# Kernel optimization log

Measured on AMD Instinct MI355X. Metric: run time of the kernel, lower is better.

Reference implementation:

```python
import jax, jax.numpy as jnp
import numpy as np

B, S, DIM, H, HD, K, DEPTH = 2, 2048, 1024, 16, 64, 64, 8
SCALE = 1.0 / np.sqrt(HD)


def _build_cantor_routes(seq_len: int, k: int, depth: int) -> np.ndarray:
    # Vectorized version of CantorAttention._build_cantor_routes
    pos = np.arange(seq_len, dtype=np.float64)
    x = pos / max(1, seq_len - 1)
    x = np.clip(x, 1e-06, 1.0 - 1e-06)
    cantor = np.zeros(seq_len, dtype=np.float64)
    factor = 0.5
    for _ in range(depth):
        x = x * 3.0
        digit = np.floor(x)
        x = x - digit
        cantor += factor * (digit == 2.0)
        factor *= 0.5
    cantor = cantor.astype(np.float32)
    # k nearest positions in Cantor space for each position
    dist = np.abs(cantor[:, None] - cantor[None, :])  # [S, S]
    routes = np.argsort(dist, axis=1, kind='stable')[:, :k]  # [S, k]
    return routes.astype(np.int32)


def setup_inputs() -> dict:
    key = jax.random.key(0)
    k1, k2, k3, k4, k5 = jax.random.split(key, 5)
    s = 1.0 / np.sqrt(DIM)
    return {
        'x': jax.random.normal(k1, (B, S, DIM), dtype=jnp.float32),
        'w_qkv': jax.random.normal(k2, (3 * DIM, DIM), dtype=jnp.float32) * s,
        'b_qkv': jax.random.normal(k3, (3 * DIM,), dtype=jnp.float32) * 0.01,
        'w_out': jax.random.normal(k4, (DIM, DIM), dtype=jnp.float32) * s,
        'b_out': jax.random.normal(k5, (DIM,), dtype=jnp.float32) * 0.01,
        'routes': jnp.asarray(_build_cantor_routes(S, K, DEPTH)),
    }


def reference(x, w_qkv, b_qkv, w_out, b_out, routes):
    b, s, _ = x.shape
    # QKV projection (torch Linear: y = x @ W.T + b)
    qkv = x @ w_qkv.T + b_qkv                       # [B, S, 3*DIM]
    qkv = qkv.reshape(b, s, 3, H, HD).transpose(2, 0, 3, 1, 4)  # [3, B, H, S, HD]
    q, k, v = qkv[0], qkv[1], qkv[2]                # each [B, H, S, HD]
    # Gather k/v at Cantor neighbor routes: [B, H, S, K, HD]
    k_g = jnp.take(k, routes, axis=2)
    v_g = jnp.take(v, routes, axis=2)
    scores = jnp.einsum('bhqd,bhqkd->bhqk', q, k_g) * SCALE
    attn = jax.nn.softmax(scores, axis=-1)
    out = jnp.einsum('bhqk,bhqkd->bhqd', attn, v_g)  # [B, H, S, HD]
    out = out.transpose(0, 2, 1, 3).reshape(b, s, DIM)
    return out @ w_out.T + b_out
```

## Files before the change

kernel.cpp:

```cpp
#include <hip/hip_runtime.h>

#define BQ   2
#define SQ   2048
#define DIMQ 1024
#define HQ   16
#define HDQ  64
#define KQ   64
#define QKV_STRIDE (3 * DIMQ)

typedef __attribute__((ext_vector_type(8))) short short8;
typedef __attribute__((ext_vector_type(4))) float floatx4;

typedef const __attribute__((address_space(1))) unsigned short* gas_t;
typedef __attribute__((address_space(3))) unsigned short* las_t;

__device__ __forceinline__ unsigned short f2b(float f) {
    union { float f; unsigned int u; } x; x.f = f;
    unsigned int r = x.u + 0x7fffu + ((x.u >> 16) & 1u);
    return (unsigned short)(r >> 16);
}
__device__ __forceinline__ float b2f(unsigned short u) {
    union { unsigned int u; float f; } x; x.u = ((unsigned int)u) << 16;
    return x.f;
}

__global__ __launch_bounds__(256) void cast3_f32_bf16(const float* __restrict__ s0, unsigned short* __restrict__ d0, int n0,
                                                      const float* __restrict__ s1, unsigned short* __restrict__ d1, int n1,
                                                      const float* __restrict__ s2, unsigned short* __restrict__ d2, int n2) {
    int i = blockIdx.x * blockDim.x + threadIdx.x;
    const float* s; unsigned short* d;
    if (i < n0)                { s = s0; d = d0; }
    else if (i < n0 + n1)      { s = s1; d = d1; i -= n0; }
    else if (i < n0 + n1 + n2) { s = s2; d = d2; i -= n0 + n1; }
    else return;
    float4 v = ((const float4*)s)[i];
    ushort4 o;
    o.x = f2b(v.x); o.y = f2b(v.y); o.z = f2b(v.z); o.w = f2b(v.w);
    ((ushort4*)d)[i] = o;
}

template <int BM, int BN, typename CT>
__global__ __launch_bounds__(256) void gemm_bf16_nt(const unsigned short* __restrict__ A,
                                                    const unsigned short* __restrict__ B,
                                                    const float* __restrict__ bias,
                                                    CT* __restrict__ C,
                                                    int M, int N, int K) {
    constexpr int MI = BM / 32;
    constexpr int NJ = BN / 32;
    __shared__ unsigned short As[BM * 64];
    __shared__ unsigned short Bs[BN * 64];

    const int tid  = threadIdx.x;
    const int lane = tid & 63;
    const int wv   = tid >> 6;
    const int wm   = (wv >> 1) * (BM / 2);
    const int wn   = (wv & 1) * (BN / 2);
    const int fr   = lane & 15;
    const int fq   = lane >> 4;

    const int m0 = blockIdx.y * BM;
    const int n0 = blockIdx.x * BN;

    floatx4 acc[MI][NJ];
#pragma unroll
    for (int i = 0; i < MI; ++i)
#pragma unroll
        for (int j = 0; j < NJ; ++j) acc[i][j] = (floatx4)(0.f);

    const unsigned short* Ab = A + (size_t)m0 * K;
    const unsigned short* Bb = B + (size_t)n0 * K;

    for (int k0 = 0; k0 < K; k0 += 64) {
#pragma unroll
        for (int c = 0; c < (BM + BN) * 8; c += 256) {
            const int cc = c + tid;
            if (cc < BM * 8) {
                const int row = cc >> 3;
                const int kc  = ((cc & 7) ^ (row & 7)) << 3;
                __builtin_amdgcn_global_load_lds(
                    (gas_t)(Ab + (size_t)row * K + k0 + kc),
                    (las_t)&As[cc * 8], 16, 0, 0);
            } else {
                const int c2  = cc - BM * 8;
                const int row = c2 >> 3;
                const int kc  = ((c2 & 7) ^ (row & 7)) << 3;
                __builtin_amdgcn_global_load_lds(
                    (gas_t)(Bb + (size_t)row * K + k0 + kc),
                    (las_t)&Bs[c2 * 8], 16, 0, 0);
            }
        }
        __syncthreads();

#pragma unroll
        for (int ks = 0; ks < 2; ++ks) {
            short8 af[MI], bf[NJ];
#pragma unroll
            for (int i = 0; i < MI; ++i) {
                const int row = wm + i * 16 + fr;
                const int pos = (ks * 4 + fq) ^ (row & 7);
                af[i] = *(const short8*)&As[row * 64 + pos * 8];
            }
#pragma unroll
            for (int j = 0; j < NJ; ++j) {
                const int row = wn + j * 16 + fr;
                const int pos = (ks * 4 + fq) ^ (row & 7);
                bf[j] = *(const short8*)&Bs[row * 64 + pos * 8];
            }
#pragma unroll
            for (int i = 0; i < MI; ++i)
#pragma unroll
                for (int j = 0; j < NJ; ++j)
                    acc[i][j] = __builtin_amdgcn_mfma_f32_16x16x32_bf16(af[i], bf[j], acc[i][j], 0, 0, 0);
        }
        __syncthreads();
    }

    float bv[NJ];
#pragma unroll
    for (int j = 0; j < NJ; ++j) bv[j] = bias[n0 + wn + j * 16 + fr];
#pragma unroll
    for (int i = 0; i < MI; ++i) {
#pragma unroll
        for (int r = 0; r < 4; ++r) {
            const size_t row = (size_t)(m0 + wm + i * 16 + fq * 4 + r);
#pragma unroll
            for (int j = 0; j < NJ; ++j) {
                const float v = acc[i][j][r] + bv[j];
                if constexpr (sizeof(CT) == 2)
                    C[row * N + n0 + wn + j * 16 + fr] = (CT)f2b(v);
                else
                    C[row * N + n0 + wn + j * 16 + fr] = (CT)v;
            }
        }
    }
}

__global__ __launch_bounds__(256) void attn_kernel(const unsigned short* __restrict__ qkv,
                                                   const int* __restrict__ routes,
                                                   unsigned short* __restrict__ out) {
    __shared__ int   r_s[KQ];
    __shared__ float m_s[128], l_s[128];
    __shared__ float o_part[8][128];

    const int t  = threadIdx.x;
    const int id = blockIdx.x;
    const int bq = (id & 7) * 512 + (id >> 3);
    const int b  = bq >> 11;
    const int q  = bq & 2047;

    if (t < KQ) r_s[t] = routes[q * KQ + t];

    const int g  = t >> 7;
    const int th = t & 127;
    const int h  = th >> 3;
    const int d0 = (t & 7) * 8;

    float qf[8];
    {
        const short8 q8 = *(const short8*)&qkv[((size_t)bq * 3) * DIMQ + h * HDQ + d0];
#pragma unroll
        for (int e = 0; e < 8; ++e) qf[e] = b2f((unsigned short)q8[e]) * 0.18033688011112042f;
    }
    __syncthreads();

    const unsigned short* baseK = qkv + ((size_t)b * SQ * 3 + 1) * DIMQ + h * HDQ + d0;
    const unsigned short* baseV = qkv + ((size_t)b * SQ * 3 + 2) * DIMQ + h * HDQ + d0;

    float s[32];
    short8 kb[4];
#pragma unroll
    for (int i = 0; i < 4; ++i) {
        const size_t roff = (size_t)r_s[i * 2 + g] * QKV_STRIDE;
        kb[i] = *(const short8*)(baseK + roff);
    }
#pragma unroll
    for (int jj = 0; jj < 32; ++jj) {
        const int slot = jj & 3;
        const short8 k8 = kb[slot];
        if (jj + 4 < 32) {
            const size_t roff = (size_t)r_s[(jj + 4) * 2 + g] * QKV_STRIDE;
            kb[slot] = *(const short8*)(baseK + roff);
        }
        float p = 0.f;
#pragma unroll
        for (int e = 0; e < 8; ++e) p += qf[e] * b2f((unsigned short)k8[e]);
        p += __shfl_xor(p, 1, 64);
        p += __shfl_xor(p, 2, 64);
        p += __shfl_xor(p, 4, 64);
        s[jj] = p;
    }

    short8 vb[4];
#pragma unroll
    for (int i = 0; i < 4; ++i) {
        const size_t roff = (size_t)r_s[i * 2 + g] * QKV_STRIDE;
        vb[i] = *(const short8*)(baseV + roff);
    }

    float mx[16];
#pragma unroll
    for (int i = 0; i < 16; ++i) mx[i] = fmaxf(s[i], s[i + 16]);
#pragma unroll
    for (int i = 0; i < 8; ++i) mx[i] = fmaxf(mx[i], mx[i + 8]);
#pragma unroll
    for (int i = 0; i < 4; ++i) mx[i] = fmaxf(mx[i], mx[i + 4]);
    const float m = fmaxf(fmaxf(mx[0], mx[1]), fmaxf(mx[2], mx[3]));

    float l0 = 0.f, l1 = 0.f, l2 = 0.f, l3 = 0.f;
#pragma unroll
    for (int jj = 0; jj < 32; jj += 4) {
        s[jj + 0] = exp2f(s[jj + 0] - m); l0 += s[jj + 0];
        s[jj + 1] = exp2f(s[jj + 1] - m); l1 += s[jj + 1];
        s[jj + 2] = exp2f(s[jj + 2] - m); l2 += s[jj + 2];
        s[jj + 3] = exp2f(s[jj + 3] - m); l3 += s[jj + 3];
    }
    const float l = (l0 + l1) + (l2 + l3);

    float o[8];
#pragma unroll
    for (int e = 0; e < 8; ++e) o[e] = 0.f;
#pragma unroll
    for (int jj = 0; jj < 32; ++jj) {
        const int slot = jj & 3;
        const short8 v8 = vb[slot];
        if (jj + 4 < 32) {
            const size_t roff = (size_t)r_s[(jj + 4) * 2 + g] * QKV_STRIDE;
            vb[slot] = *(const short8*)(baseV + roff);
        }
        const float p = s[jj];
#pragma unroll
        for (int e = 0; e < 8; ++e) o[e] += p * b2f((unsigned short)v8[e]);
    }

    if (g == 1) {
        m_s[th] = m; l_s[th] = l;
#pragma unroll
        for (int e = 0; e < 8; ++e) o_part[e][th] = o[e];
    }
    __syncthreads();
    if (g == 0) {
        const float m1 = m_s[th], l1m = l_s[th];
        const float mm = fmaxf(m, m1);
        const float a0 = exp2f(m - mm);
        const float a1 = exp2f(m1 - mm);
        const float inv = 1.0f / (l * a0 + l1m * a1);
        float oo[8];
#pragma unroll
        for (int e = 0; e < 8; ++e) oo[e] = (o[e] * a0 + o_part[e][th] * a1) * inv;
        ushort4 lo, hi;
        lo.x = f2b(oo[0]); lo.y = f2b(oo[1]); lo.z = f2b(oo[2]); lo.w = f2b(oo[3]);
        hi.x = f2b(oo[4]); hi.y = f2b(oo[5]); hi.z = f2b(oo[6]); hi.w = f2b(oo[7]);
        ushort4* dst = (ushort4*)&out[(size_t)bq * DIMQ + h * HDQ + d0];
        dst[0] = lo; dst[1] = hi;
    }
}

extern "C" void kernel_launch(void* const* d_in, const int* in_sizes, int n_in,
                              void* d_out, int out_size, void* d_ws, size_t ws_size,
                              hipStream_t stream) {
    const float* x      = (const float*)d_in[0];
    const float* w_qkv  = (const float*)d_in[1];
    const float* b_qkv  = (const float*)d_in[2];
    const float* w_out  = (const float*)d_in[3];
    const float* b_out  = (const float*)d_in[4];
    const int*   routes = (const int*)d_in[5];
    float* out = (float*)d_out;

    char* ws = (char*)d_ws;
    unsigned short* qkvb  = (unsigned short*)ws;
    unsigned short* xb    = (unsigned short*)(ws + 25165824);
    unsigned short* attnb = xb;
    unsigned short* wqb   = (unsigned short*)(ws + 33554432);
    unsigned short* wob   = (unsigned short*)(ws + 39845888);

    const int M = BQ * SQ;
    dim3 blk(256);

    {
        const int n0 = M * DIMQ / 4, n1 = 3 * DIMQ * DIMQ / 4, n2 = DIMQ * DIMQ / 4;
        cast3_f32_bf16<<<(n0 + n1 + n2 + 255) / 256, blk, 0, stream>>>(
            x, xb, n0, w_qkv, wqb, n1, w_out, wob, n2);
    }

    gemm_bf16_nt<128, 128, unsigned short><<<dim3(3 * DIMQ / 128, M / 128), blk, 0, stream>>>(
        xb, wqb, b_qkv, qkvb, M, 3 * DIMQ, DIMQ);

    attn_kernel<<<BQ * SQ, blk, 0, stream>>>(qkvb, routes, attnb);

    gemm_bf16_nt<128, 64, float><<<dim3(DIMQ / 64, M / 128), blk, 0, stream>>>(
        attnb, wob, b_out, out, M, DIMQ, DIMQ);
}
```

Before: 187.5 us.

## Stage gathered K/V rows through LDS with async global_load_lds double buffering

The register-prefetched gather of K and V rows in the attention kernel is replaced by a double-buffered pipeline built on __builtin_amdgcn_global_load_lds, which writes each wave's rows straight into a per-wave LDS staging buffer. Explicit vmcnt waits overlap the next chunk's loads with compute on the current chunk. The first V chunks are issued while the last K chunk is still being computed. This aims to hide gather latency and lower register pressure, but it uses 32KB of LDS per block, which may cut occupancy, and it relies on hand-written waitcnt ordering being correct.

Result: slower. 204.4 us (+9.1%).

```diff
diff --git a/kernel.cpp b/kernel.cpp
--- a/kernel.cpp
+++ b/kernel.cpp
@@ -141,6 +141,7 @@
     __shared__ int   r_s[KQ];
     __shared__ float m_s[128], l_s[128];
     __shared__ float o_part[8][128];
+    __shared__ __align__(16) unsigned short stage[4][2][4][512];
 
     const int t  = threadIdx.x;
     const int id = blockIdx.x;
@@ -150,10 +151,12 @@
 
     if (t < KQ) r_s[t] = routes[q * KQ + t];
 
-    const int g  = t >> 7;
-    const int th = t & 127;
-    const int h  = th >> 3;
-    const int d0 = (t & 7) * 8;
+    const int g    = t >> 7;
+    const int th   = t & 127;
+    const int h    = th >> 3;
+    const int d0   = (t & 7) * 8;
+    const int wave = t >> 6;
+    const int lane = t & 63;
 
     float qf[8];
     {
@@ -166,36 +169,52 @@
     const unsigned short* baseK = qkv + ((size_t)b * SQ * 3 + 1) * DIMQ + h * HDQ + d0;
     const unsigned short* baseV = qkv + ((size_t)b * SQ * 3 + 2) * DIMQ + h * HDQ + d0;
 
+#define ISSUE(base, c, bf) do {                                               \
+    _Pragma("unroll")                                                         \
+    for (int u = 0; u < 4; ++u) {                                             \
+        const size_t roff = (size_t)r_s[((c) * 4 + u) * 2 + g] * QKV_STRIDE;  \
+        __builtin_amdgcn_global_load_lds((gas_t)((base) + roff),              \
+            (las_t)&stage[wave][bf][u][lane * 8], 16, 0, 0);                  \
+    }                                                                         \
+} while (0)
+
+#define WAIT4 asm volatile("s_waitcnt vmcnt(4)" ::: "memory")
+#define WAIT0 asm volatile("s_waitcnt vmcnt(0)" ::: "memory")
+
+#define COMP_K(c, bf) do {                                                    \
+    _Pragma("unroll")                                                         \
+    for (int u = 0; u < 4; ++u) {                                             \
+        const short8 k8 = *(const short8*)&stage[wave][bf][u][lane * 8];      \
+        float p = 0.f;                                                        \
+        _Pragma("unroll")                                                     \
+        for (int e = 0; e < 8; ++e) p += qf[e] * b2f((unsigned short)k8[e]);  \
+        p += __shfl_xor(p, 1, 64);                                            \
+        p += __shfl_xor(p, 2, 64);                                            \
+        p += __shfl_xor(p, 4, 64);                                            \
+        s[(c) * 4 + u] = p;                                                   \
+    }                                                                         \
+} while (0)
+
+#define COMP_V(c, bf) do {                                                    \
+    _Pragma("unroll")                                                         \
+    for (int u = 0; u < 4; ++u) {                                             \
+        const short8 v8 = *(const short8*)&stage[wave][bf][u][lane * 8];      \
+        const float p = s[(c) * 4 + u];                                       \
+        _Pragma("unroll")                                                     \
+        for (int e = 0; e < 8; ++e) o[e] += p * b2f((unsigned short)v8[e]);   \
+    }                                                                         \
+} while (0)
+
     float s[32];
-    short8 kb[4];
-#pragma unroll
-    for (int i = 0; i < 4; ++i) {
-        const size_t roff = (size_t)r_s[i * 2 + g] * QKV_STRIDE;
-        kb[i] = *(const short8*)(baseK + roff);
-    }
-#pragma unroll
-    for (int jj = 0; jj < 32; ++jj) {
-        const int slot = jj & 3;
-        const short8 k8 = kb[slot];
-        if (jj + 4 < 32) {
-            const size_t roff = (size_t)r_s[(jj + 4) * 2 + g] * QKV_STRIDE;
-            kb[slot] = *(const short8*)(baseK + roff);
-        }
-        float p = 0.f;
-#pragma unroll
-        for (int e = 0; e < 8; ++e) p += qf[e] * b2f((unsigned short)k8[e]);
-        p += __shfl_xor(p, 1, 64);
-        p += __shfl_xor(p, 2, 64);
-        p += __shfl_xor(p, 4, 64);
-        s[jj] = p;
-    }
-
-    short8 vb[4];
-#pragma unroll
-    for (int i = 0; i < 4; ++i) {
-        const size_t roff = (size_t)r_s[i * 2 + g] * QKV_STRIDE;
-        vb[i] = *(const short8*)(baseV + roff);
-    }
+    ISSUE(baseK, 0, 0); ISSUE(baseK, 1, 1);
+    WAIT4; COMP_K(0, 0); ISSUE(baseK, 2, 0);
+    WAIT4; COMP_K(1, 1); ISSUE(baseK, 3, 1);
+    WAIT4; COMP_K(2, 0); ISSUE(baseK, 4, 0);
+    WAIT4; COMP_K(3, 1); ISSUE(baseK, 5, 1);
+    WAIT4; COMP_K(4, 0); ISSUE(baseK, 6, 0);
+    WAIT4; COMP_K(5, 1); ISSUE(baseK, 7, 1);
+    WAIT4; COMP_K(6, 0); ISSUE(baseV, 0, 0);
+    WAIT4; COMP_K(7, 1); ISSUE(baseV, 1, 1);
 
     float mx[16];
 #pragma unroll
@@ -219,18 +238,20 @@
     float o[8];
 #pragma unroll
     for (int e = 0; e < 8; ++e) o[e] = 0.f;
-#pragma unroll
-    for (int jj = 0; jj < 32; ++jj) {
-        const int slot = jj & 3;
-        const short8 v8 = vb[slot];
-        if (jj + 4 < 32) {
-            const size_t roff = (size_t)r_s[(jj + 4) * 2 + g] * QKV_STRIDE;
-            vb[slot] = *(const short8*)(baseV + roff);
-        }
-        const float p = s[jj];
-#pragma unroll
-        for (int e = 0; e < 8; ++e) o[e] += p * b2f((unsigned short)v8[e]);
-    }
+    WAIT4; COMP_V(0, 0); ISSUE(baseV, 2, 0);
+    WAIT4; COMP_V(1, 1); ISSUE(baseV, 3, 1);
+    WAIT4; COMP_V(2, 0); ISSUE(baseV, 4, 0);
+    WAIT4; COMP_V(3, 1); ISSUE(baseV, 5, 1);
+    WAIT4; COMP_V(4, 0); ISSUE(baseV, 6, 0);
+    WAIT4; COMP_V(5, 1); ISSUE(baseV, 7, 1);
+    WAIT4; COMP_V(6, 0);
+    WAIT0; COMP_V(7, 1);
+
+#undef ISSUE
+#undef WAIT4
+#undef WAIT0
+#undef COMP_K
+#undef COMP_V
 
     if (g == 1) {
         m_s[th] = m; l_s[th] = l;
```
